# Performance work log

Hardware: AMD Instinct MI355X
Metric: run time of the kernel (lower is better)

Reference implementation:

```python
import jax, jax.numpy as jnp
import numpy as np

H = 4096      # hidden_size
NH = 32       # num heads
HD = H // NH  # head_dim = 128
I = 11008     # intermediate_size
T = 2048      # num tokens (single prompt sequence)
G = 128       # AWQ group size
EPS = 1e-6
ROPE_BASE = 10000.0


def _make_qlinear(key, k_in, n_out):
    k1, k2, k3 = jax.random.split(key, 3)
    qw = jax.random.randint(k1, (k_in, n_out), 0, 16, dtype=jnp.int32)
    qz = jax.random.randint(k2, (k_in // G, n_out), 0, 16, dtype=jnp.int32)
    scales = jax.random.uniform(k3, (k_in // G, n_out), dtype=jnp.float32) * 0.01 + 1e-3
    return qw, scales, qz


def setup_inputs() -> dict:
    key = jax.random.key(0)
    ks = jax.random.split(key, 8)
    inp = {
        "positions": jnp.arange(T, dtype=jnp.int64),
        "hidden_states": jax.random.normal(ks[0], (T, H), dtype=jnp.float32),
        "input_ln_w": jnp.ones((H,), dtype=jnp.float32),
        "post_ln_w": jnp.ones((H,), dtype=jnp.float32),
    }
    inp["qkv_qw"], inp["qkv_scales"], inp["qkv_qz"] = _make_qlinear(ks[1], H, 3 * H)
    inp["o_qw"], inp["o_scales"], inp["o_qz"] = _make_qlinear(ks[2], H, H)
    inp["gu_qw"], inp["gu_scales"], inp["gu_qz"] = _make_qlinear(ks[3], H, 2 * I)
    inp["down_qw"], inp["down_scales"], inp["down_qz"] = _make_qlinear(ks[4], I, H)
    return inp


def rms_norm(x, w):
    var = jnp.mean(x * x, axis=-1, keepdims=True)
    return x * jax.lax.rsqrt(var + EPS) * w


def awq_linear(x, qw, scales, qz):
    # dequant: (q - z) * scale, group-wise along K; then dense GEMM
    w = (qw.astype(scales.dtype) - jnp.repeat(qz.astype(scales.dtype), G, axis=0)) \
        * jnp.repeat(scales, G, axis=0)
    return x @ w


def apply_rope(x, positions):
    # x: [T, NH, HD], neox-style half rotation, rotary_dim = HD
    inv_freq = 1.0 / (ROPE_BASE ** (jnp.arange(0, HD, 2, dtype=jnp.float32) / HD))
    ang = positions.astype(jnp.float32)[:, None] * inv_freq  # [T, HD/2]
    cos = jnp.cos(ang)[:, None, :]
    sin = jnp.sin(ang)[:, None, :]
    x1, x2 = x[..., : HD // 2], x[..., HD // 2:]
    return jnp.concatenate([x1 * cos - x2 * sin, x2 * cos + x1 * sin], axis=-1)


def reference(positions, hidden_states, input_ln_w, post_ln_w,
              qkv_qw, qkv_scales, qkv_qz, o_qw, o_scales, o_qz,
              gu_qw, gu_scales, gu_qz, down_qw, down_scales, down_qz):
    residual = hidden_states
    x = rms_norm(hidden_states, input_ln_w)

    # attention
    qkv = awq_linear(x, qkv_qw, qkv_scales, qkv_qz)  # [T, 3H]
    q, k, v = jnp.split(qkv, 3, axis=-1)
    q = apply_rope(q.reshape(T, NH, HD), positions)
    k = apply_rope(k.reshape(T, NH, HD), positions)
    v = v.reshape(T, NH, HD)
    scale = HD ** -0.5
    scores = jnp.einsum('qhd,khd->hqk', q, k) * scale  # [NH, T, T]
    causal = jnp.tril(jnp.ones((T, T), dtype=bool))
    scores = jnp.where(causal[None], scores, jnp.finfo(scores.dtype).min)
    probs = jax.nn.softmax(scores, axis=-1)
    attn = jnp.einsum('hqk,khd->qhd', probs, v).reshape(T, H)
    attn_out = awq_linear(attn, o_qw, o_scales, o_qz)

    hidden = residual + attn_out
    residual = hidden
    x = rms_norm(hidden, post_ln_w)

    # MLP: gate_up -> silu(gate) * up -> down
    gate_up = awq_linear(x, gu_qw, gu_scales, gu_qz)  # [T, 2I]
    gate, up = jnp.split(gate_up, 2, axis=-1)
    x = jax.nn.silu(gate) * up
    x = awq_linear(x, down_qw, down_scales, down_qz)
    return residual + x
```

## Files before the change

kernel.cpp:

```cpp
#include <hip/hip_runtime.h>
#include <stdint.h>

#define T_SEQ 2048
#define HID 4096
#define NHEADS 32
#define I_FF 11008
#define QKV_N 12288
#define GU_N 22016

typedef unsigned short u16;
typedef unsigned int u32;
typedef __attribute__((ext_vector_type(4))) float f32x4;
typedef __attribute__((ext_vector_type(8))) __bf16 bf16x8;
typedef __attribute__((ext_vector_type(4))) u32 u32x4;
typedef __attribute__((ext_vector_type(2))) u32 u32x2;

__device__ __forceinline__ u16 f2bf(float f) {
  union { float f; u32 u; } v; v.f = f;
  u32 u = v.u;
  return (u16)((u + 0x7fffu + ((u >> 16) & 1u)) >> 16);
}
__device__ __forceinline__ float bf2f(u16 h) {
  union { u32 u; float f; } v; v.u = ((u32)h) << 16;
  return v.f;
}
__device__ __forceinline__ void split2(float x, u16& hi, u16& lo) {
  hi = f2bf(x);
  lo = f2bf(x - bf2f(hi));
}
__device__ __forceinline__ void split8(const float* v, u32x4& H, u32x4& L) {
#pragma unroll
  for (int j = 0; j < 4; j++) {
    u16 h0, l0, h1, l1;
    split2(v[2 * j], h0, l0);
    split2(v[2 * j + 1], h1, l1);
    H[j] = (u32)h0 | ((u32)h1 << 16);
    L[j] = (u32)l0 | ((u32)l1 << 16);
  }
}
__device__ __forceinline__ void dq8(u32 rbp, int zq, u32x4& w) {
#pragma unroll
  for (int j = 0; j < 4; j++) {
    int q0 = (int)((rbp >> (8 * j)) & 15u) - zq;
    int q1 = (int)((rbp >> (8 * j + 4)) & 15u) - zq;
    u32 b0 = __builtin_bit_cast(u32, (float)q0);
    u32 b1 = __builtin_bit_cast(u32, (float)q1);
    w[j] = __builtin_amdgcn_perm(b1, b0, 0x07060302u);
  }
}

__global__ __launch_bounds__(256) void pack_qw_kernel(
    const int* __restrict__ qw, u32* __restrict__ pw, int N) {
  int n = blockIdx.x * 256 + threadIdx.x;
  int oct = blockIdx.y;
  const int* src = qw + (size_t)oct * 8 * N + n;
  u32 v = 0;
#pragma unroll
  for (int j = 0; j < 8; j++)
    v |= ((u32)src[(size_t)j * N] & 15u) << (4 * j);
  pw[(size_t)oct * N + n] = v;
}

__global__ __launch_bounds__(256) void rmsnorm_kernel(
    const float* __restrict__ in, const float* __restrict__ w,
    u16* __restrict__ outh) {
  int row = blockIdx.x;
  const float* x = in + (size_t)row * HID;
  float4 vals[4];
  float ss = 0.f;
#pragma unroll
  for (int k = 0; k < 4; k++) {
    vals[k] = ((const float4*)x)[threadIdx.x + k * 256];
    ss += vals[k].x * vals[k].x + vals[k].y * vals[k].y +
          vals[k].z * vals[k].z + vals[k].w * vals[k].w;
  }
#pragma unroll
  for (int o = 1; o < 64; o <<= 1) ss += __shfl_xor(ss, o);
  __shared__ float red[4];
  if ((threadIdx.x & 63) == 0) red[threadIdx.x >> 6] = ss;
  __syncthreads();
  ss = red[0] + red[1] + red[2] + red[3];
  float rs = rsqrtf(ss * (1.f / HID) + 1e-6f);
#pragma unroll
  for (int k = 0; k < 4; k++) {
    int c4 = threadIdx.x + k * 256;
    float4 wv = ((const float4*)w)[c4];
    float o[4] = {vals[k].x * rs * wv.x, vals[k].y * rs * wv.y,
                  vals[k].z * rs * wv.z, vals[k].w * rs * wv.w};
    u32x2 H;
    H[0] = (u32)f2bf(o[0]) | ((u32)f2bf(o[1]) << 16);
    H[1] = (u32)f2bf(o[2]) | ((u32)f2bf(o[3]) << 16);
    *(u32x2*)(outh + (size_t)row * HID + c4 * 4) = H;
  }
}

template <bool RESID, bool OUTBF16>
__global__ __launch_bounds__(512) void awq_gemm256_kernel(
    const u16* __restrict__ Ahg,
    const u32* __restrict__ pw, const float* __restrict__ scales,
    const int* __restrict__ qz, const float* __restrict__ resid,
    void* __restrict__ outp, int N, int K, int nstrips) {
  __shared__ u16 AhL[2][128][40];
  __shared__ u16 BqL[2][256][40];
  int tid = threadIdx.x;
  int lane = tid & 63;
  int wid = tid >> 6;
  int g16 = lane >> 4, l16 = lane & 15;
  int p = blockIdx.x;
  int xcd = p & 7;
  int idx = p >> 3;
  int s = idx >> 1;
  int mi = ((idx & 1) << 3) + xcd;
  if (s >= nstrips) return;
  int m0 = mi * 128;
  int n0 = s * 256;
  int wr = wid >> 2, wc = wid & 3;

  f32x4 acc[4][4] = {};
  float svold[4];

  int a_row = tid >> 2, a_kc = (tid & 3) * 8;
  const u16* aph = Ahg + (size_t)(m0 + a_row) * K + a_kc;
  int b_n = tid & 255;
  int b_oct = (tid >> 8) * 2;
  int b_kb = b_oct * 8;
  const u32* pwp = pw + (size_t)b_oct * N + n0 + b_n;
  const float* scp = scales + n0;
  const int* qzp = qz + n0 + b_n;

  int nsteps = K >> 5;

  u32x4 rah;
  u32 rb0, rb1;

  auto load_step = [&](int ks) {
    int k0 = ks << 5;
    rah = *(const u32x4*)(aph + k0);
    const u32* q = pwp + (size_t)(ks << 2) * N;
    rb0 = q[0];
    rb1 = q[N];
  };
  auto write_step = [&](int buf, int zq) {
    *(u32x4*)&AhL[buf][a_row][a_kc] = rah;
    u32x4 w0, w1;
    dq8(rb0, zq, w0);
    dq8(rb1, zq, w1);
    *(u32x4*)&BqL[buf][b_n][b_kb] = w0;
    *(u32x4*)&BqL[buf][b_n][b_kb + 8] = w1;
  };

  int zq = qzp[0];
  load_step(0);
  write_step(0, zq);
#pragma unroll
  for (int n = 0; n < 4; n++)
    svold[n] = scp[wc * 64 + n * 16 + l16];
  __syncthreads();

  int cur = 0;
  for (int ks = 0; ks < nsteps; ks++) {
    int nxt = ks + 1;
    if (nxt < nsteps) {
      if ((nxt & 3) == 0) zq = qzp[(size_t)(nxt >> 2) * N];
      load_step(nxt);
    }
    if (ks != 0 && (ks & 3) == 0) {
      int g = ks >> 2;
#pragma unroll
      for (int n = 0; n < 4; n++) {
        float svnew = scp[(size_t)g * N + wc * 64 + n * 16 + l16];
        float r = svold[n] * __builtin_amdgcn_rcpf(svnew);
        svold[n] = svnew;
#pragma unroll
        for (int m = 0; m < 4; m++)
#pragma unroll
          for (int i = 0; i < 4; i++) acc[m][n][i] *= r;
      }
    }
    bf16x8 bq[4];
#pragma unroll
    for (int n = 0; n < 4; n++)
      bq[n] = __builtin_bit_cast(bf16x8,
          *(const u32x4*)&BqL[cur][wc * 64 + n * 16 + l16][g16 * 8]);
    __builtin_amdgcn_s_setprio(1);
#pragma unroll
    for (int m = 0; m < 4; m++) {
      bf16x8 ah = __builtin_bit_cast(bf16x8,
          *(const u32x4*)&AhL[cur][wr * 64 + m * 16 + l16][g16 * 8]);
#pragma unroll
      for (int n = 0; n < 4; n++)
        acc[m][n] = __builtin_amdgcn_mfma_f32_16x16x32_bf16(ah, bq[n], acc[m][n], 0, 0, 0);
    }
    __builtin_amdgcn_s_setprio(0);
    if (nxt < nsteps) write_step(cur ^ 1, zq);
    __syncthreads();
    cur ^= 1;
  }
#pragma unroll
  for (int n = 0; n < 4; n++)
#pragma unroll
    for (int m = 0; m < 4; m++)
#pragma unroll
      for (int i = 0; i < 4; i++) acc[m][n][i] *= svold[n];
#pragma unroll
  for (int m = 0; m < 4; m++) {
#pragma unroll
    for (int n = 0; n < 4; n++) {
#pragma unroll
      for (int r = 0; r < 4; r++) {
        int row = m0 + wr * 64 + m * 16 + g16 * 4 + r;
        int col = n0 + wc * 64 + n * 16 + l16;
        float v = acc[m][n][r];
        if (RESID) v += resid[(size_t)row * N + col];
        if (OUTBF16)
          ((u16*)outp)[(size_t)row * N + col] = f2bf(v);
        else
          ((float*)outp)[(size_t)row * N + col] = v;
      }
    }
  }
}

__global__ __launch_bounds__(256) void rope_kernel(float* __restrict__ qkv) {
  int t = blockIdx.x;
  __shared__ float cs[64], sn[64];
  if (threadIdx.x < 64) {
    int i = threadIdx.x;
    float freq = exp2f(-(float)i * (13.287712379549449f / 64.f));
    float ang = (float)t * freq;
    cs[i] = cosf(ang);
    sn[i] = sinf(ang);
  }
  __syncthreads();
#pragma unroll
  for (int it = 0; it < 16; it++) {
    int idx = threadIdx.x + it * 256;
    int part = idx >> 11;
    int rem = idx & 2047;
    int hh = rem >> 6, i = rem & 63;
    float* base = qkv + (size_t)t * QKV_N + (size_t)part * HID + hh * 128;
    float x1 = base[i], x2 = base[64 + i];
    float c = cs[i], s = sn[i];
    base[i] = x1 * c - x2 * s;
    base[64 + i] = x2 * c + x1 * s;
  }
}

__global__ __launch_bounds__(256) void transpose_v_kernel(
    const float* __restrict__ qkv, u16* __restrict__ vt) {
  __shared__ u16 tile[64][65];
  int tb = blockIdx.x;
  int cb = blockIdx.y;
  int tid = threadIdx.x;
  int r = tid >> 2, c16 = (tid & 3) * 16;
  const float* src = qkv + (size_t)(tb * 64 + r) * QKV_N + 2 * HID + cb * 64 + c16;
  float v[16];
  *(float4*)&v[0] = *(const float4*)(src);
  *(float4*)&v[4] = *(const float4*)(src + 4);
  *(float4*)&v[8] = *(const float4*)(src + 8);
  *(float4*)&v[12] = *(const float4*)(src + 12);
#pragma unroll
  for (int i = 0; i < 16; i++) tile[r][c16 + i] = f2bf(v[i]);
  __syncthreads();
  int ocol = tid >> 2, tchunk = (tid & 3) * 16;
  u16 vbuf[16];
#pragma unroll
  for (int i = 0; i < 16; i++) vbuf[i] = tile[tchunk + i][ocol];
  u16* dst = vt + (size_t)(cb * 64 + ocol) * T_SEQ + tb * 64 + tchunk;
  *(u32x4*)dst = *(u32x4*)&vbuf[0];
  *(u32x4*)(dst + 8) = *(u32x4*)&vbuf[8];
}

__global__ __launch_bounds__(256) void attn_kernel(
    const float* __restrict__ qkv, const u16* __restrict__ vt,
    u16* __restrict__ outh) {
  constexpr float SCALE = 0.08838834764831845f;
  __shared__ u16 Kh[32][136], Kl[32][136];
  __shared__ u16 Vt_lds[128][40];
  __shared__ u16 P_lds[4][16][40];
  int tid = threadIdx.x;
  int wid = tid >> 6, lane = tid & 63;
  int g16 = lane >> 4, l16 = lane & 15;
  int h = blockIdx.x & 31;
  int qt = blockIdx.x >> 5;
  int qb = qt * 64;

  bf16x8 qh[4], ql[4];
  {
    const float* qsrc = qkv + (size_t)(qb + wid * 16 + l16) * QKV_N + h * 128;
#pragma unroll
    for (int ds = 0; ds < 4; ds++) {
      float v[8];
      *(float4*)&v[0] = *(const float4*)(qsrc + ds * 32 + g16 * 8);
      *(float4*)&v[4] = *(const float4*)(qsrc + ds * 32 + g16 * 8 + 4);
      u32x4 H, L;
      split8(v, H, L);
      qh[ds] = __builtin_bit_cast(bf16x8, H);
      ql[ds] = __builtin_bit_cast(bf16x8, L);
    }
  }
  f32x4 oacc[8] = {};
  float mrun[4] = {-1e30f, -1e30f, -1e30f, -1e30f};
  float lrun[4] = {0.f, 0.f, 0.f, 0.f};

  int st_k = tid >> 3, st_d = (tid & 7) * 16;
  int sv_d = tid >> 1, sv_k = (tid & 1) * 16;

  int ktiles = (qb + 64) >> 5;
  for (int kt = 0; kt < ktiles; kt++) {
    __syncthreads();
    {
      const float* src = qkv + (size_t)(kt * 32 + st_k) * QKV_N + HID + h * 128 + st_d;
      float v[16];
      *(float4*)&v[0] = *(const float4*)(src);
      *(float4*)&v[4] = *(const float4*)(src + 4);
      *(float4*)&v[8] = *(const float4*)(src + 8);
      *(float4*)&v[12] = *(const float4*)(src + 12);
      u32x4 H, L;
      split8(&v[0], H, L);
      *(u32x4*)&Kh[st_k][st_d] = H;
      *(u32x4*)&Kl[st_k][st_d] = L;
      split8(&v[8], H, L);
      *(u32x4*)&Kh[st_k][st_d + 8] = H;
      *(u32x4*)&Kl[st_k][st_d + 8] = L;
    }
    {
      const u16* src = vt + (size_t)(h * 128 + sv_d) * T_SEQ + kt * 32 + sv_k;
      *(u32x4*)&Vt_lds[sv_d][sv_k] = *(const u32x4*)src;
      *(u32x4*)&Vt_lds[sv_d][sv_k + 8] = *(const u32x4*)(src + 8);
    }
    __syncthreads();
    f32x4 sacc[2] = {};
#pragma unroll
    for (int kb = 0; kb < 2; kb++)
#pragma unroll
      for (int ds = 0; ds < 4; ds++) {
        bf16x8 kfh = __builtin_bit_cast(bf16x8,
            *(const u32x4*)&Kh[kb * 16 + l16][ds * 32 + g16 * 8]);
        bf16x8 kfl = __builtin_bit_cast(bf16x8,
            *(const u32x4*)&Kl[kb * 16 + l16][ds * 32 + g16 * 8]);
        sacc[kb] = __builtin_amdgcn_mfma_f32_16x16x32_bf16(qh[ds], kfh, sacc[kb], 0, 0, 0);
        sacc[kb] = __builtin_amdgcn_mfma_f32_16x16x32_bf16(ql[ds], kfh, sacc[kb], 0, 0, 0);
        sacc[kb] = __builtin_amdgcn_mfma_f32_16x16x32_bf16(qh[ds], kfl, sacc[kb], 0, 0, 0);
      }
    float p0v[4], p1v[4];
#pragma unroll
    for (int r = 0; r < 4; r++) {
      int qrow = qb + wid * 16 + g16 * 4 + r;
      bool msk0 = (kt * 32 + l16) > qrow;
      bool msk1 = (kt * 32 + 16 + l16) > qrow;
      float s0 = msk0 ? -1e30f : sacc[0][r] * SCALE;
      float s1 = msk1 ? -1e30f : sacc[1][r] * SCALE;
      float tm = fmaxf(s0, s1);
      tm = fmaxf(tm, __shfl_xor(tm, 1));
      tm = fmaxf(tm, __shfl_xor(tm, 2));
      tm = fmaxf(tm, __shfl_xor(tm, 4));
      tm = fmaxf(tm, __shfl_xor(tm, 8));
      float mnew = fmaxf(mrun[r], tm);
      float fac = __expf(mrun[r] - mnew);
      float p0 = msk0 ? 0.f : __expf(s0 - mnew);
      float p1 = msk1 ? 0.f : __expf(s1 - mnew);
      float ts = p0 + p1;
      ts += __shfl_xor(ts, 1);
      ts += __shfl_xor(ts, 2);
      ts += __shfl_xor(ts, 4);
      ts += __shfl_xor(ts, 8);
      lrun[r] = lrun[r] * fac + ts;
      mrun[r] = mnew;
      p0v[r] = p0; p1v[r] = p1;
#pragma unroll
      for (int db = 0; db < 8; db++) oacc[db][r] *= fac;
    }
#pragma unroll
    for (int r = 0; r < 4; r++) {
      P_lds[wid][g16 * 4 + r][l16] = f2bf(p0v[r]);
      P_lds[wid][g16 * 4 + r][16 + l16] = f2bf(p1v[r]);
    }
    __syncthreads();
    bf16x8 pa = __builtin_bit_cast(bf16x8, *(const u32x4*)&P_lds[wid][l16][g16 * 8]);
#pragma unroll
    for (int db = 0; db < 8; db++) {
      bf16x8 vb = __builtin_bit_cast(bf16x8,
          *(const u32x4*)&Vt_lds[db * 16 + l16][g16 * 8]);
      oacc[db] = __builtin_amdgcn_mfma_f32_16x16x32_bf16(pa, vb, oacc[db], 0, 0, 0);
    }
  }
#pragma unroll
  for (int r = 0; r < 4; r++) {
    int qrow = qb + wid * 16 + g16 * 4 + r;
    float inv = 1.f / lrun[r];
#pragma unroll
    for (int db = 0; db < 8; db++)
      outh[(size_t)qrow * HID + h * 128 + db * 16 + l16] =
          f2bf(oacc[db][r] * inv);
  }
}

__global__ __launch_bounds__(256) void silu_mul_kernel(
    const u16* __restrict__ gu, u16* __restrict__ acth) {
  size_t e = ((size_t)blockIdx.x * 256 + threadIdx.x) * 8;
  size_t row = e / I_FF;
  int col = (int)(e % I_FF);
  const u16* gp = gu + row * GU_N + col;
  u32x4 gv = *(const u32x4*)gp;
  u32x4 uv = *(const u32x4*)(gp + I_FF);
  u32x4 H;
#pragma unroll
  for (int j = 0; j < 4; j++) {
    float g0 = bf2f((u16)(gv[j] & 0xffff)), g1 = bf2f((u16)(gv[j] >> 16));
    float u0 = bf2f((u16)(uv[j] & 0xffff)), u1 = bf2f((u16)(uv[j] >> 16));
    float o0 = g0 / (1.f + __expf(-g0)) * u0;
    float o1 = g1 / (1.f + __expf(-g1)) * u1;
    H[j] = (u32)f2bf(o0) | ((u32)f2bf(o1) << 16);
  }
  *(u32x4*)(acth + row * I_FF + col) = H;
}

extern "C" void kernel_launch(void* const* d_in, const int* in_sizes, int n_in,
                              void* d_out, int out_size, void* d_ws, size_t ws_size,
                              hipStream_t stream) {
  const float* hs    = (const float*)d_in[1];
  const float* ln1   = (const float*)d_in[2];
  const float* ln2   = (const float*)d_in[3];
  const int* qkv_qw  = (const int*)d_in[4];
  const float* qkv_s = (const float*)d_in[5];
  const int* qkv_z   = (const int*)d_in[6];
  const int* o_qw    = (const int*)d_in[7];
  const float* o_s   = (const float*)d_in[8];
  const int* o_z     = (const int*)d_in[9];
  const int* gu_qw   = (const int*)d_in[10];
  const float* gu_s  = (const float*)d_in[11];
  const int* gu_z    = (const int*)d_in[12];
  const int* dn_qw   = (const int*)d_in[13];
  const float* dn_s  = (const float*)d_in[14];
  const int* dn_z    = (const int*)d_in[15];

  char* ws = (char*)d_ws;
  u16*   xnh    = (u16*)(ws);
  float* qkv    = (float*)(ws + (size_t)33554432);
  u16*   vt     = (u16*)(ws + (size_t)134217728);
  float* hidden = (float*)(ws + (size_t)150994944);
  u16*   gup    = (u16*)(ws + (size_t)184549376);
  u16*   attnh  = xnh;
  u16*   acth   = (u16*)qkv;
  u32* pk_gup = (u32*)gup;
  u32* pk_qkv = (u32*)((char*)qkv + (size_t)50331648);

  auto grid256 = [](int N) { return 16 * (N / 256); };

  rmsnorm_kernel<<<T_SEQ, 256, 0, stream>>>(hs, ln1, xnh);
  pack_qw_kernel<<<dim3(QKV_N / 256, HID / 8), 256, 0, stream>>>(qkv_qw, pk_gup, QKV_N);
  awq_gemm256_kernel<false, false><<<grid256(QKV_N), 512, 0, stream>>>(
      xnh, pk_gup, qkv_s, qkv_z, nullptr, qkv, QKV_N, HID, QKV_N / 256);
  rope_kernel<<<T_SEQ, 256, 0, stream>>>(qkv);
  transpose_v_kernel<<<dim3(T_SEQ / 64, HID / 64), 256, 0, stream>>>(qkv, vt);
  attn_kernel<<<NHEADS * (T_SEQ / 64), 256, 0, stream>>>(qkv, vt, attnh);
  pack_qw_kernel<<<dim3(HID / 256, HID / 8), 256, 0, stream>>>(o_qw, pk_gup, HID);
  awq_gemm256_kernel<true, false><<<grid256(HID), 512, 0, stream>>>(
      attnh, pk_gup, o_s, o_z, hs, hidden, HID, HID, HID / 256);
  rmsnorm_kernel<<<T_SEQ, 256, 0, stream>>>(hidden, ln2, xnh);
  pack_qw_kernel<<<dim3(GU_N / 256, HID / 8), 256, 0, stream>>>(gu_qw, pk_qkv, GU_N);
  awq_gemm256_kernel<false, true><<<grid256(GU_N), 512, 0, stream>>>(
      xnh, pk_qkv, gu_s, gu_z, nullptr, gup, GU_N, HID, GU_N / 256);
  silu_mul_kernel<<<(T_SEQ * (size_t)I_FF / 8 / 256), 256, 0, stream>>>(gup, acth);
  pack_qw_kernel<<<dim3(HID / 256, I_FF / 8), 256, 0, stream>>>(dn_qw, pk_gup, HID);
  awq_gemm256_kernel<true, false><<<grid256(HID), 512, 0, stream>>>(
      acth, pk_gup, dn_s, dn_z, hidden, (float*)d_out, HID, I_FF, HID / 256);
}
```

Before: 1.583 ms.

## Prepack AWQ weights as zero-subtracted FP8 bytes and dequant from LDS

The pack kernel now folds the zero point into each weight and stores (q - z) as an FP8 E4M3 byte, which is exact for integers in [-15,15]. The GEMM then loads FP8 bytes, stages them in LDS at half the previous footprint, and converts to bf16 with hardware pk_f32_fp8 and cvt_pk_bf16 instructions just before the MFMA. This drops the per-step zero-point loads and the integer-to-float dequant on the write path. In exchange it doubles the packed weight buffer compared with the int4 format and moves the conversion into the inner loop, where each wave now repeats it.

```diff
diff --git a/kernel.cpp b/kernel.cpp
--- a/kernel.cpp
+++ b/kernel.cpp
@@ -10,7 +10,9 @@
 
 typedef unsigned short u16;
 typedef unsigned int u32;
+typedef unsigned char u8;
 typedef __attribute__((ext_vector_type(4))) float f32x4;
+typedef __attribute__((ext_vector_type(2))) float f32x2;
 typedef __attribute__((ext_vector_type(8))) __bf16 bf16x8;
 typedef __attribute__((ext_vector_type(4))) u32 u32x4;
 typedef __attribute__((ext_vector_type(2))) u32 u32x2;
@@ -38,27 +40,48 @@
     L[j] = (u32)l0 | ((u32)l1 << 16);
   }
 }
-__device__ __forceinline__ void dq8(u32 rbp, int zq, u32x4& w) {
-#pragma unroll
-  for (int j = 0; j < 4; j++) {
-    int q0 = (int)((rbp >> (8 * j)) & 15u) - zq;
-    int q1 = (int)((rbp >> (8 * j + 4)) & 15u) - zq;
-    u32 b0 = __builtin_bit_cast(u32, (float)q0);
-    u32 b1 = __builtin_bit_cast(u32, (float)q1);
-    w[j] = __builtin_amdgcn_perm(b1, b0, 0x07060302u);
-  }
-}
-
-__global__ __launch_bounds__(256) void pack_qw_kernel(
-    const int* __restrict__ qw, u32* __restrict__ pw, int N) {
+__device__ __forceinline__ bf16x8 dqf8(u32x2 v) {
+  u32x4 w;
+#pragma unroll
+  for (int i = 0; i < 2; i++) {
+    f32x2 lo = __builtin_amdgcn_cvt_pk_f32_fp8(v[i], false);
+    f32x2 hi = __builtin_amdgcn_cvt_pk_f32_fp8(v[i], true);
+    u32 r0, r1;
+    asm("v_cvt_pk_bf16_f32 %0, %1, %2" : "=v"(r0) : "v"(lo[0]), "v"(lo[1]));
+    asm("v_cvt_pk_bf16_f32 %0, %1, %2" : "=v"(r1) : "v"(hi[0]), "v"(hi[1]));
+    w[2 * i] = r0;
+    w[2 * i + 1] = r1;
+  }
+  return __builtin_bit_cast(bf16x8, w);
+}
+
+__global__ __launch_bounds__(256) void pack_fp8_kernel(
+    const int* __restrict__ qw, const int* __restrict__ qz,
+    u32* __restrict__ pw8, int N) {
   int n = blockIdx.x * 256 + threadIdx.x;
-  int oct = blockIdx.y;
-  const int* src = qw + (size_t)oct * 8 * N + n;
-  u32 v = 0;
-#pragma unroll
-  for (int j = 0; j < 8; j++)
-    v |= ((u32)src[(size_t)j * N] & 15u) << (4 * j);
-  pw[(size_t)oct * N + n] = v;
+  int op = blockIdx.y;
+  int zq = qz[(size_t)(op >> 3) * N + n];
+  const int* src = qw + (size_t)op * 16 * N + n;
+  u32x4 out;
+#pragma unroll
+  for (int w = 0; w < 4; w++) {
+    u32 acc = 0;
+#pragma unroll
+    for (int b = 0; b < 4; b++) {
+      int v = src[(size_t)(w * 4 + b) * N] - zq;
+      u32 byte = 0;
+      if (v != 0) {
+        u32 u = __builtin_bit_cast(u32, (float)v);
+        u32 s = u >> 31;
+        u32 E = (u >> 23) & 255u;
+        u32 m3 = (u >> 20) & 7u;
+        byte = (s << 7) | ((E - 120u) << 3) | m3;
+      }
+      acc |= byte << (8 * b);
+    }
+    out[w] = acc;
+  }
+  *(u32x4*)(pw8 + ((size_t)op * N + n) * 4) = out;
 }
 
 __global__ __launch_bounds__(256) void rmsnorm_kernel(
@@ -95,13 +118,13 @@
 }
 
 template <bool RESID, bool OUTBF16>
-__global__ __launch_bounds__(512) void awq_gemm256_kernel(
+__global__ __launch_bounds__(512) void awq_gemm256f_kernel(
     const u16* __restrict__ Ahg,
-    const u32* __restrict__ pw, const float* __restrict__ scales,
-    const int* __restrict__ qz, const float* __restrict__ resid,
+    const u32* __restrict__ pw8, const float* __restrict__ scales,
+    const float* __restrict__ resid,
     void* __restrict__ outp, int N, int K, int nstrips) {
   __shared__ u16 AhL[2][128][40];
-  __shared__ u16 BqL[2][256][40];
+  __shared__ __align__(16) u8 BqL8[2][256][48];
   int tid = threadIdx.x;
   int lane = tid & 63;
   int wid = tid >> 6;
@@ -122,36 +145,25 @@
   int a_row = tid >> 2, a_kc = (tid & 3) * 8;
   const u16* aph = Ahg + (size_t)(m0 + a_row) * K + a_kc;
   int b_n = tid & 255;
-  int b_oct = (tid >> 8) * 2;
-  int b_kb = b_oct * 8;
-  const u32* pwp = pw + (size_t)b_oct * N + n0 + b_n;
+  int b_p = tid >> 8;
+  const u32* pwp = pw8 + ((size_t)b_p * N + n0 + b_n) * 4;
   const float* scp = scales + n0;
-  const int* qzp = qz + n0 + b_n;
 
   int nsteps = K >> 5;
 
-  u32x4 rah;
-  u32 rb0, rb1;
+  u32x4 rah, rb;
 
   auto load_step = [&](int ks) {
-    int k0 = ks << 5;
-    rah = *(const u32x4*)(aph + k0);
-    const u32* q = pwp + (size_t)(ks << 2) * N;
-    rb0 = q[0];
-    rb1 = q[N];
+    rah = *(const u32x4*)(aph + (ks << 5));
+    rb = *(const u32x4*)(pwp + (size_t)(ks << 1) * N * 4);
   };
-  auto write_step = [&](int buf, int zq) {
+  auto write_step = [&](int buf) {
     *(u32x4*)&AhL[buf][a_row][a_kc] = rah;
-    u32x4 w0, w1;
-    dq8(rb0, zq, w0);
-    dq8(rb1, zq, w1);
-    *(u32x4*)&BqL[buf][b_n][b_kb] = w0;
-    *(u32x4*)&BqL[buf][b_n][b_kb + 8] = w1;
+    *(u32x4*)&BqL8[buf][b_n][b_p * 16] = rb;
   };
 
-  int zq = qzp[0];
   load_step(0);
-  write_step(0, zq);
+  write_step(0);
 #pragma unroll
   for (int n = 0; n < 4; n++)
     svold[n] = scp[wc * 64 + n * 16 + l16];
@@ -160,10 +172,7 @@
   int cur = 0;
   for (int ks = 0; ks < nsteps; ks++) {
     int nxt = ks + 1;
-    if (nxt < nsteps) {
-      if ((nxt & 3) == 0) zq = qzp[(size_t)(nxt >> 2) * N];
-      load_step(nxt);
-    }
+    if (nxt < nsteps) load_step(nxt);
     if (ks != 0 && (ks & 3) == 0) {
       int g = ks >> 2;
 #pragma unroll
@@ -179,9 +188,10 @@
     }
     bf16x8 bq[4];
 #pragma unroll
-    for (int n = 0; n < 4; n++)
-      bq[n] = __builtin_bit_cast(bf16x8,
-          *(const u32x4*)&BqL[cur][wc * 64 + n * 16 + l16][g16 * 8]);
+    for (int n = 0; n < 4; n++) {
+      u32x2 b8 = *(const u32x2*)&BqL8[cur][wc * 64 + n * 16 + l16][g16 * 8];
+      bq[n] = dqf8(b8);
+    }
     __builtin_amdgcn_s_setprio(1);
 #pragma unroll
     for (int m = 0; m < 4; m++) {
@@ -192,7 +202,7 @@
         acc[m][n] = __builtin_amdgcn_mfma_f32_16x16x32_bf16(ah, bq[n], acc[m][n], 0, 0, 0);
     }
     __builtin_amdgcn_s_setprio(0);
-    if (nxt < nsteps) write_step(cur ^ 1, zq);
+    if (nxt < nsteps) write_step(cur ^ 1);
     __syncthreads();
     cur ^= 1;
   }
@@ -444,26 +454,26 @@
   u16*   attnh  = xnh;
   u16*   acth   = (u16*)qkv;
   u32* pk_gup = (u32*)gup;
-  u32* pk_qkv = (u32*)((char*)qkv + (size_t)50331648);
+  u32* pk_qkv = (u32*)qkv;
 
   auto grid256 = [](int N) { return 16 * (N / 256); };
 
   rmsnorm_kernel<<<T_SEQ, 256, 0, stream>>>(hs, ln1, xnh);
-  pack_qw_kernel<<<dim3(QKV_N / 256, HID / 8), 256, 0, stream>>>(qkv_qw, pk_gup, QKV_N);
-  awq_gemm256_kernel<false, false><<<grid256(QKV_N), 512, 0, stream>>>(
-      xnh, pk_gup, qkv_s, qkv_z, nullptr, qkv, QKV_N, HID, QKV_N / 256);
+  pack_fp8_kernel<<<dim3(QKV_N / 256, HID / 16), 256, 0, stream>>>(qkv_qw, qkv_z, pk_gup, QKV_N);
+  awq_gemm256f_kernel<false, false><<<grid256(QKV_N), 512, 0, stream>>>(
+      xnh, pk_gup, qkv_s, nullptr, qkv, QKV_N, HID, QKV_N / 256);
   rope_kernel<<<T_SEQ, 256, 0, stream>>>(qkv);
   transpose_v_kernel<<<dim3(T_SEQ / 64, HID / 64), 256, 0, stream>>>(qkv, vt);
   attn_kernel<<<NHEADS * (T_SEQ / 64), 256, 0, stream>>>(qkv, vt, attnh);
-  pack_qw_kernel<<<dim3(HID / 256, HID / 8), 256, 0, stream>>>(o_qw, pk_gup, HID);
-  awq_gemm256_kernel<true, false><<<grid256(HID), 512, 0, stream>>>(
-      attnh, pk_gup, o_s, o_z, hs, hidden, HID, HID, HID / 256);
+  pack_fp8_kernel<<<dim3(HID / 256, HID / 16), 256, 0, stream>>>(o_qw, o_z, pk_gup, HID);
+  awq_gemm256f_kernel<true, false><<<grid256(HID), 512, 0, stream>>>(
+      attnh, pk_gup, o_s, hs, hidden, HID, HID, HID / 256);
   rmsnorm_kernel<<<T_SEQ, 256, 0, stream>>>(hidden, ln2, xnh);
-  pack_qw_kernel<<<dim3(GU_N / 256, HID / 8), 256, 0, stream>>>(gu_qw, pk_qkv, GU_N);
-  awq_gemm256_kernel<false, true><<<grid256(GU_N), 512, 0, stream>>>(
-      xnh, pk_qkv, gu_s, gu_z, nullptr, gup, GU_N, HID, GU_N / 256);
+  pack_fp8_kernel<<<dim3(GU_N / 256, HID / 16), 256, 0, stream>>>(gu_qw, gu_z, pk_qkv, GU_N);
+  awq_gemm256f_kernel<false, true><<<grid256(GU_N), 512, 0, stream>>>(
+      xnh, pk_qkv, gu_s, nullptr, gup, GU_N, HID, GU_N / 256);
   silu_mul_kernel<<<(T_SEQ * (size_t)I_FF / 8 / 256), 256, 0, stream>>>(gup, acth);
-  pack_qw_kernel<<<dim3(HID / 256, I_FF / 8), 256, 0, stream>>>(dn_qw, pk_gup, HID);
-  awq_gemm256_kernel<true, false><<<grid256(HID), 512, 0, stream>>>(
-      acth, pk_gup, dn_s, dn_z, hidden, (float*)d_out, HID, I_FF, HID / 256);
-}
+  pack_fp8_kernel<<<dim3(HID / 256, I_FF / 16), 256, 0, stream>>>(dn_qw, dn_z, pk_gup, HID);
+  awq_gemm256f_kernel<true, false><<<grid256(HID), 512, 0, stream>>>(
+      acth, pk_gup, dn_s, hidden, (float*)d_out, HID, I_FF, HID / 256);
+}
```

After: 1.593 ms. About the same (+0.6%).
